# Kernel optimization log

Measured on AMD Instinct MI355X. Metric: run time of the kernel, lower is better.

The kernel has to match this reference:

```python
import jax, jax.numpy as jnp
import numpy as np

B, T, D = 16, 4096, 512
GROUP, TECH, FINAL = 5, 10, 25
# ownership maps (each level's indices are partitioned by the parent class)
# group_to_tech_map = {0:[0],1:[1],2:[2,3,4],3:[5,6,7],4:[8,9]}
TECH_OWNER = np.array([0, 1, 2, 2, 2, 3, 3, 3, 4, 4], dtype=np.int32)
# tech_to_final_tech_map inverted: final index -> owning tech index
FINAL_OWNER = np.zeros(FINAL, dtype=np.int32)
for t, idxs in {0:[0],1:[1,19],2:[2,3,4],3:[5,6,7,8,9,10,11,12,20,21,22,24],4:[13],5:[17],6:[15],7:[18],8:[16],9:[14,23]}.items():
    for i in idxs:
        FINAL_OWNER[i] = t
TECH_OWNER = jnp.asarray(TECH_OWNER)
FINAL_OWNER = jnp.asarray(FINAL_OWNER)


def upsample_nearest(z, out_size):
    # z: [B, T, C] -> [B, out_size, C]; torch nn.Upsample(mode='nearest') on the time axis
    t = z.shape[1]
    idx = (jnp.arange(out_size) * t) // out_size
    return z[:, idx, :]


def setup_inputs() -> dict:
    key = jax.random.key(0)
    ks = jax.random.split(key, 7)
    s = 1.0 / np.sqrt(D)
    return {
        "x": jax.random.normal(ks[0], (B, T, D), dtype=jnp.float32),
        "Wg": jax.random.uniform(ks[1], (D, GROUP), jnp.float32, -s, s),
        "bg": jax.random.uniform(ks[2], (GROUP,), jnp.float32, -s, s),
        "Wt": jax.random.uniform(ks[3], (D, TECH), jnp.float32, -s, s),
        "bt": jax.random.uniform(ks[4], (TECH,), jnp.float32, -s, s),
        "Wf": jax.random.uniform(ks[5], (D, FINAL), jnp.float32, -s, s),
        "bf": jax.random.uniform(ks[6], (FINAL,), jnp.float32, -s, s),
        "note_size": 8192,
    }


def reference(x, Wg, bg, Wt, bt, Wf, bf, note_size):
    # dropout is identity at inference
    group_logits = jnp.einsum('btd,dg->btg', x, Wg) + bg          # [B,T,5]
    group_pred = jnp.argmax(group_logits, axis=-1)                 # [B,T]
    tech_out = jnp.einsum('btd,dk->btk', x, Wt) + bt               # [B,T,10]
    # masked scatter-add loop == ownership mask (maps partition the indices)
    tech_mask = (group_pred[..., None] == TECH_OWNER[None, None, :])
    tech_logits = tech_out * tech_mask.astype(tech_out.dtype)
    tech_pred = jnp.argmax(tech_logits, axis=-1)                   # [B,T]
    final_out = jnp.einsum('btd,df->btf', x, Wf) + bf              # [B,T,25]
    final_mask = (tech_pred[..., None] == FINAL_OWNER[None, None, :])
    final_tech_logits = final_out * final_mask.astype(final_out.dtype)
    frame_level_final_tech_logits = final_tech_logits
    group_up = upsample_nearest(group_logits, note_size)
    tech_up = upsample_nearest(tech_logits, note_size)
    final_up = upsample_nearest(final_tech_logits, note_size)
    return (group_up, tech_up, final_up, frame_level_final_tech_logits)
```

## Files before the change

kernel.cpp:

```cpp
#include <hip/hip_runtime.h>
#include <stdint.h>

#define NB 16
#define NTF 4096
#define ND 512
#define NS 8192
#define NCOL 40
#define ROWSB 64
#define BLOCK 512
#define NWAVE 8
#define CPW 5
#define CD 32
#define NCH 16
#define LGS 65

typedef float v4f  __attribute__((ext_vector_type(4)));
typedef float v16f __attribute__((ext_vector_type(16)));

extern "C" __global__ void pack_w_kernel(const float* __restrict__ Wg,
                                         const float* __restrict__ Wt,
                                         const float* __restrict__ Wf,
                                         float* __restrict__ Wp3)
{
    int o = blockIdx.x * 256 + threadIdx.x;
    if (o >= NCOL * ND) return;
    int s20 = o / 20, r = o % 20;
    int c = r >> 2, dl = r & 3;
    int u = s20 >> 3, w = s20 & 7;
    int d = u * 4 + dl, col = w * 5 + c;
    float v;
    if (col < 5)       v = Wg[d * 5  + col];
    else if (col < 15) v = Wt[d * 10 + (col - 5)];
    else               v = Wf[d * 25 + (col - 15)];
    Wp3[o] = v;
}

#define GLDS(gp, lp) __builtin_amdgcn_global_load_lds( \
    (const __attribute__((address_space(1))) unsigned int*)(gp), \
    (__attribute__((address_space(3))) unsigned int*)(lp), 16, 0, 0)

#define WEL(C16, C4, c, dl) \
    ((4*(c)+(dl)) < 16 ? (C16)[4*(c)+(dl)] : (C4)[4*(c)+(dl)-16])

#define SUB(S, C16, C4, N16, N4, PF) do {                                     \
    asm volatile("s_waitcnt lgkmcnt(0)" : "+s"(C16), "+s"(C4) :: "memory");   \
    if (PF) {                                                                 \
        asm volatile("s_load_dwordx16 %0, %2, %3\n\t"                         \
                     "s_load_dwordx4 %1, %2, %4"                              \
            : "=s"(N16), "=s"(N4)                                             \
            : "s"(wch + ((((S)+1) >> 3) * 1280)),                             \
              "i"((((S)+1) & 7) * 640), "i"(((((S)+1) & 7) * 640) + 64));     \
    }                                                                         \
    v4f xcur = xnext;                                                         \
    if ((S) < 7) xnext = *(const v4f*)(xb + (((S)+1)*64 + lane) * 4);         \
    _Pragma("unroll")                                                         \
    for (int c = 0; c < CPW; ++c) {                                           \
        float a = acc[c];                                                     \
        a = fmaf(xcur.x, WEL(C16, C4, c, 0), a);                              \
        a = fmaf(xcur.y, WEL(C16, C4, c, 1), a);                              \
        a = fmaf(xcur.z, WEL(C16, C4, c, 2), a);                              \
        a = fmaf(xcur.w, WEL(C16, C4, c, 3), a);                              \
        acc[c] = a;                                                           \
    }                                                                         \
} while (0)

extern "C" __global__ void __launch_bounds__(BLOCK, 8)
hier_main(const float* __restrict__ x,
          const float* __restrict__ bg, const float* __restrict__ bt,
          const float* __restrict__ bf,
          const float* __restrict__ Wp3, float* __restrict__ out)
{
    __shared__ __align__(16) float xs[3][ROWSB * CD];
    __shared__ float Lg[NCOL * LGS];

    const int t    = threadIdx.x;
    const int lane = t & 63;
    const int w    = t >> 6;
    const int row0 = blockIdx.x * ROWSB;

    const int wu    = __builtin_amdgcn_readfirstlane(w);
    const int ldsof = wu * 1024;
    const float* Wp3w = Wp3 + wu * 20;

    float acc[CPW];
#pragma unroll
    for (int c = 0; c < CPW; ++c) acc[c] = 0.f;

    auto stage = [&](int ch_, int p_) {
        const float* gp = x + (size_t)(row0 + lane) * ND + ch_ * CD + w * 4;
        GLDS(gp, (char*)&xs[p_][0] + ldsof);
    };

    v16f bA16, bB16;
    v4f  bA4,  bB4;

    stage(0, 0);
    stage(1, 1);
    asm volatile("s_load_dwordx16 %0, %2, 0\n\t"
                 "s_load_dwordx4 %1, %2, 64"
                 : "=s"(bA16), "=s"(bA4) : "s"(Wp3w));

    int pc = 0;
    for (int ch = 0; ch < NCH; ++ch) {
        if (ch < NCH - 1) asm volatile("s_waitcnt vmcnt(1)" ::: "memory");
        else              asm volatile("s_waitcnt vmcnt(0)" ::: "memory");
        __builtin_amdgcn_s_barrier();
        __builtin_amdgcn_sched_barrier(0);
        if (ch < NCH - 2) {
            int ps = pc + 2; if (ps >= 3) ps -= 3;
            stage(ch + 2, ps);
        }
        __builtin_amdgcn_sched_barrier(0);

        const float* xb  = &xs[pc][0];
        const float* wch = Wp3w + (size_t)ch * 1280;
        v4f xnext = *(const v4f*)(xb + lane * 4);

        const bool pf7 = (ch < NCH - 1);
        SUB(0, bA16, bA4, bB16, bB4, true);
        SUB(1, bB16, bB4, bA16, bA4, true);
        SUB(2, bA16, bA4, bB16, bB4, true);
        SUB(3, bB16, bB4, bA16, bA4, true);
        SUB(4, bA16, bA4, bB16, bB4, true);
        SUB(5, bB16, bB4, bA16, bA4, true);
        SUB(6, bA16, bA4, bB16, bB4, true);
        SUB(7, bB16, bB4, bA16, bA4, pf7);

        pc = (pc + 1 == 3) ? 0 : pc + 1;
    }

#pragma unroll
    for (int c = 0; c < CPW; ++c) Lg[(w * CPW + c) * LGS + lane] = acc[c];
    __syncthreads();

    if (t < 64) {
        constexpr int TOWN[10] = {0,1,2,2,2,3,3,3,4,4};
        constexpr int FOWN[25] = {0,1,2,2,2,3,3,3,3,3,3,3,3,4,9,6,8,5,7,1,3,3,3,9,3};
        const int r = t;
        float gl[5]; int gp = 0; float gbest = -INFINITY;
#pragma unroll
        for (int c = 0; c < 5; ++c) {
            float v = Lg[c * LGS + r] + bg[c];
            gl[c] = v;
            if (v > gbest) { gbest = v; gp = c; }
        }
        float tl[10]; int tp = 0; float tbest = -INFINITY;
#pragma unroll
        for (int k = 0; k < 10; ++k) {
            float v = (Lg[(5 + k) * LGS + r] + bt[k]) * ((TOWN[k] == gp) ? 1.f : 0.f);
            tl[k] = v;
            if (v > tbest) { tbest = v; tp = k; }
        }
#pragma unroll
        for (int c = 0; c < 5; ++c)  Lg[c * LGS + r] = gl[c];
#pragma unroll
        for (int k = 0; k < 10; ++k) Lg[(5 + k) * LGS + r] = tl[k];
#pragma unroll
        for (int f = 0; f < 25; ++f) {
            float v = (Lg[(15 + f) * LGS + r] + bf[f]) * ((FOWN[f] == tp) ? 1.f : 0.f);
            Lg[(15 + f) * LGS + r] = v;
        }
    }
    __syncthreads();

    const int b   = row0 >> 12;
    const int tt0 = row0 & (NTF - 1);

    {
        float* og = out + ((size_t)b * NS + 2 * (size_t)tt0) * 5;
        for (int i = t; i < 640; i += BLOCK) {
            int s = i / 5, c = i - s * 5;
            og[i] = Lg[c * LGS + (s >> 1)];
        }
    }
    {
        float* ot = out + (size_t)NB * NS * 5 + ((size_t)b * NS + 2 * (size_t)tt0) * 10;
        for (int i = t; i < 1280; i += BLOCK) {
            int s = i / 10, c = i - s * 10;
            ot[i] = Lg[(5 + c) * LGS + (s >> 1)];
        }
    }
    {
        float* of = out + (size_t)NB * NS * 15 + ((size_t)b * NS + 2 * (size_t)tt0) * 25;
        for (int i = t; i < 3200; i += BLOCK) {
            int s = i / 25, c = i - s * 25;
            of[i] = Lg[(15 + c) * LGS + (s >> 1)];
        }
    }
    {
        float* ofr = out + (size_t)NB * NS * 40 + ((size_t)b * NTF + tt0) * 25;
        for (int i = t; i < 1600; i += BLOCK) {
            int s = i / 25, c = i - s * 25;
            ofr[i] = Lg[(15 + c) * LGS + s];
        }
    }
}

extern "C" void kernel_launch(void* const* d_in, const int* in_sizes, int n_in,
                              void* d_out, int out_size, void* d_ws, size_t ws_size,
                              hipStream_t stream)
{
    const float* x  = (const float*)d_in[0];
    const float* Wg = (const float*)d_in[1];
    const float* bg = (const float*)d_in[2];
    const float* Wt = (const float*)d_in[3];
    const float* bt = (const float*)d_in[4];
    const float* Wf = (const float*)d_in[5];
    const float* bf = (const float*)d_in[6];
    float* Wp3  = (float*)d_ws;
    float* outp = (float*)d_out;

    hipLaunchKernelGGL(pack_w_kernel, dim3((NCOL * ND + 255) / 256), dim3(256), 0, stream,
                       Wg, Wt, Wf, Wp3);
    hipLaunchKernelGGL(hier_main, dim3((NB * NTF) / ROWSB), dim3(BLOCK), 0, stream,
                       x, bg, bt, bf, Wp3, outp);
}
```

Baseline: 57.48 us.

## Process two rows per thread to amortize scalar weight loads

Doubles the rows per block from 64 to 128 so each thread accumulates two rows, sharing every scalar-loaded weight element between two FMA chains. Each LDS staging step now issues two async global-to-LDS loads per thread, so the wait count rises to vmcnt(2). The epilogue loops and LDS logit buffer are resized to match. This halves the grid and raises LDS and register use per block, which may cut the number of resident blocks per CU and reduce latency hiding.

After: 64.54 us. 1.12x slower.

```diff
diff --git a/kernel.cpp b/kernel.cpp
--- a/kernel.cpp
+++ b/kernel.cpp
@@ -6,13 +6,12 @@
 #define ND 512
 #define NS 8192
 #define NCOL 40
-#define ROWSB 64
+#define ROWSB 128
 #define BLOCK 512
-#define NWAVE 8
 #define CPW 5
 #define CD 32
 #define NCH 16
-#define LGS 65
+#define LGS 132
 
 typedef float v4f  __attribute__((ext_vector_type(4)));
 typedef float v16f __attribute__((ext_vector_type(16)));
@@ -51,20 +50,27 @@
             : "s"(wch + ((((S)+1) >> 3) * 1280)),                             \
               "i"((((S)+1) & 7) * 640), "i"(((((S)+1) & 7) * 640) + 64));     \
     }                                                                         \
-    v4f xcur = xnext;                                                         \
-    if ((S) < 7) xnext = *(const v4f*)(xb + (((S)+1)*64 + lane) * 4);         \
+    v4f xc0 = xn0, xc1 = xn1;                                                 \
+    if ((S) < 7) {                                                            \
+        xn0 = *(const v4f*)(xb + (size_t)(((S)+1)*128 + lane) * 4);           \
+        xn1 = *(const v4f*)(xb + (size_t)(((S)+1)*128 + 64 + lane) * 4);      \
+    }                                                                         \
     _Pragma("unroll")                                                         \
     for (int c = 0; c < CPW; ++c) {                                           \
-        float a = acc[c];                                                     \
-        a = fmaf(xcur.x, WEL(C16, C4, c, 0), a);                              \
-        a = fmaf(xcur.y, WEL(C16, C4, c, 1), a);                              \
-        a = fmaf(xcur.z, WEL(C16, C4, c, 2), a);                              \
-        a = fmaf(xcur.w, WEL(C16, C4, c, 3), a);                              \
-        acc[c] = a;                                                           \
+        float a0 = acc0[c], a1 = acc1[c];                                     \
+        a0 = fmaf(xc0.x, WEL(C16, C4, c, 0), a0);                             \
+        a1 = fmaf(xc1.x, WEL(C16, C4, c, 0), a1);                             \
+        a0 = fmaf(xc0.y, WEL(C16, C4, c, 1), a0);                             \
+        a1 = fmaf(xc1.y, WEL(C16, C4, c, 1), a1);                             \
+        a0 = fmaf(xc0.z, WEL(C16, C4, c, 2), a0);                             \
+        a1 = fmaf(xc1.z, WEL(C16, C4, c, 2), a1);                             \
+        a0 = fmaf(xc0.w, WEL(C16, C4, c, 3), a0);                             \
+        a1 = fmaf(xc1.w, WEL(C16, C4, c, 3), a1);                             \
+        acc0[c] = a0; acc1[c] = a1;                                           \
     }                                                                         \
 } while (0)
 
-extern "C" __global__ void __launch_bounds__(BLOCK, 8)
+extern "C" __global__ void __launch_bounds__(BLOCK, 4)
 hier_main(const float* __restrict__ x,
           const float* __restrict__ bg, const float* __restrict__ bt,
           const float* __restrict__ bf,
@@ -78,17 +84,22 @@
     const int w    = t >> 6;
     const int row0 = blockIdx.x * ROWSB;
 
-    const int wu    = __builtin_amdgcn_readfirstlane(w);
-    const int ldsof = wu * 1024;
+    const int wu      = __builtin_amdgcn_readfirstlane(w);
     const float* Wp3w = Wp3 + wu * 20;
 
-    float acc[CPW];
-#pragma unroll
-    for (int c = 0; c < CPW; ++c) acc[c] = 0.f;
+    float acc0[CPW], acc1[CPW];
+#pragma unroll
+    for (int c = 0; c < CPW; ++c) { acc0[c] = 0.f; acc1[c] = 0.f; }
 
     auto stage = [&](int ch_, int p_) {
-        const float* gp = x + (size_t)(row0 + lane) * ND + ch_ * CD + w * 4;
-        GLDS(gp, (char*)&xs[p_][0] + ldsof);
+#pragma unroll
+        for (int k = 0; k < 2; ++k) {
+            const int j  = w + k * 8;
+            const int dq = j >> 1;
+            const int rh = j & 1;
+            const float* gp = x + (size_t)(row0 + rh * 64 + lane) * ND + ch_ * CD + dq * 4;
+            GLDS(gp, (char*)&xs[p_][0] + (size_t)j * 1024);
+        }
     };
 
     v16f bA16, bB16;
@@ -102,7 +113,7 @@
 
     int pc = 0;
     for (int ch = 0; ch < NCH; ++ch) {
-        if (ch < NCH - 1) asm volatile("s_waitcnt vmcnt(1)" ::: "memory");
+        if (ch < NCH - 1) asm volatile("s_waitcnt vmcnt(2)" ::: "memory");
         else              asm volatile("s_waitcnt vmcnt(0)" ::: "memory");
         __builtin_amdgcn_s_barrier();
         __builtin_amdgcn_sched_barrier(0);
@@ -114,7 +125,8 @@
 
         const float* xb  = &xs[pc][0];
         const float* wch = Wp3w + (size_t)ch * 1280;
-        v4f xnext = *(const v4f*)(xb + lane * 4);
+        v4f xn0 = *(const v4f*)(xb + (size_t)lane * 4);
+        v4f xn1 = *(const v4f*)(xb + (size_t)(64 + lane) * 4);
 
         const bool pf7 = (ch < NCH - 1);
         SUB(0, bA16, bA4, bB16, bB4, true);
@@ -130,10 +142,13 @@
     }
 
 #pragma unroll
-    for (int c = 0; c < CPW; ++c) Lg[(w * CPW + c) * LGS + lane] = acc[c];
+    for (int c = 0; c < CPW; ++c) {
+        Lg[(w * CPW + c) * LGS + lane]      = acc0[c];
+        Lg[(w * CPW + c) * LGS + 64 + lane] = acc1[c];
+    }
     __syncthreads();
 
-    if (t < 64) {
+    if (t < ROWSB) {
         constexpr int TOWN[10] = {0,1,2,2,2,3,3,3,4,4};
         constexpr int FOWN[25] = {0,1,2,2,2,3,3,3,3,3,3,3,3,4,9,6,8,5,7,1,3,3,3,9,3};
         const int r = t;
@@ -168,28 +183,28 @@
 
     {
         float* og = out + ((size_t)b * NS + 2 * (size_t)tt0) * 5;
-        for (int i = t; i < 640; i += BLOCK) {
+        for (int i = t; i < 1280; i += BLOCK) {
             int s = i / 5, c = i - s * 5;
             og[i] = Lg[c * LGS + (s >> 1)];
         }
     }
     {
         float* ot = out + (size_t)NB * NS * 5 + ((size_t)b * NS + 2 * (size_t)tt0) * 10;
-        for (int i = t; i < 1280; i += BLOCK) {
+        for (int i = t; i < 2560; i += BLOCK) {
             int s = i / 10, c = i - s * 10;
             ot[i] = Lg[(5 + c) * LGS + (s >> 1)];
         }
     }
     {
         float* of = out + (size_t)NB * NS * 15 + ((size_t)b * NS + 2 * (size_t)tt0) * 25;
-        for (int i = t; i < 3200; i += BLOCK) {
+        for (int i = t; i < 6400; i += BLOCK) {
             int s = i / 25, c = i - s * 25;
             of[i] = Lg[(15 + c) * LGS + (s >> 1)];
         }
     }
     {
         float* ofr = out + (size_t)NB * NS * 40 + ((size_t)b * NTF + tt0) * 25;
-        for (int i = t; i < 1600; i += BLOCK) {
+        for (int i = t; i < 3200; i += BLOCK) {
             int s = i / 25, c = i - s * 25;
             ofr[i] = Lg[(15 + c) * LGS + s];
         }
```
